# Kernel tuning notes

Measured on AMD Instinct MI355X. Metric: run time of the kernel, lower is better.

The kernel has to match this reference:

```python
import jax, jax.numpy as jnp
import numpy as np
from itertools import combinations

# Static conv hyperparameters (match init_kwargs)
KH = KW = 3
SH = SW = 1
PH = PW = 1
DH = DW = 1
MAJ_DIM = 3  # = kernel_size[0]


def _maj_sim(x):
    """Vectorized bipolar majority-gate simulation. x: [B, n] -> [B].
    result = sum over majority subsets of prod((1+x)_in, (1-x)_out) / 2^(n-1) - 1
    """
    n = x.shape[1]
    thresh = (n + 1) // 2
    one_plus = 1.0 + x
    one_minus = 1.0 - x
    res = jnp.zeros(x.shape[0], dtype=x.dtype)
    for k in range(thresh, n + 1):
        for combo in combinations(range(n), k):
            mask = np.zeros(n, dtype=bool)
            mask[list(combo)] = True
            res = res + jnp.prod(jnp.where(jnp.asarray(mask), one_plus, one_minus), axis=1)
    return res / (2.0 ** (n - 1)) - 1.0


def _stack_maj_sim(x, maj_dim):
    """Stacked majority tree reduction along dim 1. x: [B, n] -> [B, n_final]."""
    B = x.shape[0]
    while x.shape[1] >= maj_dim:
        num_chunks = x.shape[1] // maj_dim
        if num_chunks == 0:
            break
        z = x[:, : num_chunks * maj_dim].reshape(B * num_chunks, maj_dim)
        x = _maj_sim(z).reshape(B, num_chunks)
    return x


def _unfold(x):
    """torch.nn.functional.unfold equivalent. x:[N,C,H,W] -> [N, C*KH*KW, L].
    Feature ordering matches torch: c-major, then kernel row, then kernel col."""
    N, C, H, W = x.shape
    H_out = (H + 2 * PH - DH * (KH - 1) - 1) // SH + 1
    W_out = (W + 2 * PW - DW * (KW - 1) - 1) // SW + 1
    xp = jnp.pad(x, ((0, 0), (0, 0), (PH, PH), (PW, PW)))
    slabs = [
        xp[:, :, i * DH : i * DH + SH * (H_out - 1) + 1 : SH,
              j * DW : j * DW + SW * (W_out - 1) + 1 : SW]
        for i in range(KH) for j in range(KW)
    ]
    p = jnp.stack(slabs, axis=2)  # [N, C, KH*KW, H_out, W_out]
    return p.reshape(N, C * KH * KW, H_out * W_out)


def setup_inputs() -> dict:
    key = jax.random.key(0)
    k1, k2 = jax.random.split(key)
    x = jax.random.normal(k1, (2, 27, 64, 64), dtype=jnp.float32)
    # kaiming-uniform-ish scale for fan_in = 27*3*3 = 243
    weight = jax.random.normal(k2, (32, 27, 3, 3), dtype=jnp.float32) * 0.06
    return {"x": x, "weight": weight}


def reference(x, weight):
    N, C, H, W = x.shape
    OC = weight.shape[0]
    H_out = (H + 2 * PH - DH * (KH - 1) - 1) // SH + 1
    W_out = (W + 2 * PW - DW * (KW - 1) - 1) // SW + 1
    patches = _unfold(x)                       # [N, F, L], F = C*KH*KW
    weight_flat = weight.reshape(OC, -1)       # [OC, F]
    # prod: [N, OC, F, L]
    prod = patches[:, None, :, :] * weight_flat[None, :, :, None]
    F_ = prod.shape[2]
    L = prod.shape[3]
    # reduce the feature dim via stacked majority simulation
    z = prod.transpose(0, 1, 3, 2).reshape(N * OC * L, F_)
    out = _stack_maj_sim(z, MAJ_DIM)           # [N*OC*L, 1]
    return out.reshape(N, OC, H_out, W_out)
```

## Files before the change

### kernel.cpp

```cpp
#include <hip/hip_runtime.h>

#define TW 16
#define TH 16
#define CIN 27
#define HH 64
#define WW 64
#define OC 32

__device__ __forceinline__ float maj3(float a, float b, float c) {
    return 0.5f * (a + b + c - a * b * c);
}

__global__ __launch_bounds__(256) void sconv_maj_kernel(
    const float* __restrict__ x,
    const float* __restrict__ wgt,
    float* __restrict__ out)
{
    __shared__ float sx[CIN][TH + 2][TW + 2];
    __shared__ float sw[CIN * 9];

    const int tx = threadIdx.x;
    const int ty = threadIdx.y;
    const int tid = ty * TW + tx;
    const int tile_w0 = blockIdx.x * TW;
    const int tile_h0 = blockIdx.y * TH;
    const int noc = blockIdx.z;
    const int n  = noc >> 5;
    const int oc = noc & 31;

    if (tid < CIN * 9)
        sw[tid] = wgt[oc * (CIN * 9) + tid];

    const int TOT = CIN * (TH + 2) * (TW + 2);
    const float* xn = x + (size_t)n * (CIN * HH * WW);
    for (int idx = tid; idx < TOT; idx += TH * TW) {
        int c   = idx / ((TH + 2) * (TW + 2));
        int rem = idx - c * ((TH + 2) * (TW + 2));
        int r   = rem / (TW + 2);
        int col = rem - r * (TW + 2);
        int gr = tile_h0 + r - 1;
        int gc = tile_w0 + col - 1;
        float v = 0.0f;
        if (gr >= 0 && gr < HH && gc >= 0 && gc < WW)
            v = xn[c * (HH * WW) + gr * WW + gc];
        ((float*)sx)[idx] = v;
    }
    __syncthreads();

    float m2[CIN];
    #pragma unroll
    for (int c = 0; c < CIN; ++c) {
        float m1[3];
        #pragma unroll
        for (int ki = 0; ki < 3; ++ki) {
            float p0 = sx[c][ty + ki][tx + 0] * sw[c * 9 + ki * 3 + 0];
            float p1 = sx[c][ty + ki][tx + 1] * sw[c * 9 + ki * 3 + 1];
            float p2 = sx[c][ty + ki][tx + 2] * sw[c * 9 + ki * 3 + 2];
            m1[ki] = maj3(p0, p1, p2);
        }
        m2[c] = maj3(m1[0], m1[1], m1[2]);
    }
    float m3[9];
    #pragma unroll
    for (int g = 0; g < 9; ++g)
        m3[g] = maj3(m2[3 * g], m2[3 * g + 1], m2[3 * g + 2]);
    float m4a = maj3(m3[0], m3[1], m3[2]);
    float m4b = maj3(m3[3], m3[4], m3[5]);
    float m4c = maj3(m3[6], m3[7], m3[8]);
    float res = maj3(m4a, m4b, m4c);

    const int h = tile_h0 + ty;
    const int w = tile_w0 + tx;
    out[(((size_t)n * OC + oc) * HH + h) * WW + w] = res;
}

extern "C" void kernel_launch(void* const* d_in, const int* in_sizes, int n_in,
                              void* d_out, int out_size, void* d_ws, size_t ws_size,
                              hipStream_t stream) {
    const float* x   = (const float*)d_in[0];
    const float* wgt = (const float*)d_in[1];
    float* out = (float*)d_out;

    dim3 block(TW, TH, 1);
    dim3 grid(WW / TW, HH / TH, 2 * OC);
    sconv_maj_kernel<<<grid, block, 0, stream>>>(x, wgt, out);
}
```

Before: 84.47 us.

## Compute two adjacent outputs per thread with float2 loads and direct weight reads

Each thread now computes two horizontally adjacent outputs, so the block shrinks to 128 threads. Overlapping window values are reused from float2 shared-memory loads and the result is written with one float2 store. Weights are read straight from global memory (uniform across the block, likely scalar loads) instead of being staged in shared memory. The aim is fewer LDS reads per output and less work per output. The cost is more registers per thread (float2 m2[27]) and half as many threads per block, which lowers latency hiding. The float2 read of prow[tx+1] at row offset 2*tx+2 relies on an even row stride of 18 floats for alignment, which holds.

```diff
diff --git a/kernel.cpp b/kernel.cpp
--- a/kernel.cpp
+++ b/kernel.cpp
@@ -1,39 +1,37 @@
 #include <hip/hip_runtime.h>
 
-#define TW 16
-#define TH 16
 #define CIN 27
 #define HH 64
 #define WW 64
 #define OC 32
+#define TW 16
+#define TH 16
 
-__device__ __forceinline__ float maj3(float a, float b, float c) {
-    return 0.5f * (a + b + c - a * b * c);
+__device__ __forceinline__ float2 pk_maj3(float2 a, float2 b, float2 c) {
+    float2 r;
+    r.x = 0.5f * (a.x + b.x + c.x - a.x * b.x * c.x);
+    r.y = 0.5f * (a.y + b.y + c.y - a.y * b.y * c.y);
+    return r;
 }
 
-__global__ __launch_bounds__(256) void sconv_maj_kernel(
+__global__ __launch_bounds__(128) void sconv_maj_kernel(
     const float* __restrict__ x,
     const float* __restrict__ wgt,
     float* __restrict__ out)
 {
     __shared__ float sx[CIN][TH + 2][TW + 2];
-    __shared__ float sw[CIN * 9];
 
     const int tx = threadIdx.x;
     const int ty = threadIdx.y;
-    const int tid = ty * TW + tx;
+    const int tid = ty * 8 + tx;
     const int tile_w0 = blockIdx.x * TW;
     const int tile_h0 = blockIdx.y * TH;
-    const int noc = blockIdx.z;
-    const int n  = noc >> 5;
-    const int oc = noc & 31;
-
-    if (tid < CIN * 9)
-        sw[tid] = wgt[oc * (CIN * 9) + tid];
+    const int n  = blockIdx.z >> 5;
+    const int oc = blockIdx.z & 31;
 
     const int TOT = CIN * (TH + 2) * (TW + 2);
     const float* xn = x + (size_t)n * (CIN * HH * WW);
-    for (int idx = tid; idx < TOT; idx += TH * TW) {
+    for (int idx = tid; idx < TOT; idx += 128) {
         int c   = idx / ((TH + 2) * (TW + 2));
         int rem = idx - c * ((TH + 2) * (TW + 2));
         int r   = rem / (TW + 2);
@@ -47,31 +45,40 @@
     }
     __syncthreads();
 
-    float m2[CIN];
+    const float* __restrict__ wb = wgt + oc * (CIN * 9);
+
+    float2 m2[CIN];
     #pragma unroll
     for (int c = 0; c < CIN; ++c) {
-        float m1[3];
+        float2 m1[3];
         #pragma unroll
         for (int ki = 0; ki < 3; ++ki) {
-            float p0 = sx[c][ty + ki][tx + 0] * sw[c * 9 + ki * 3 + 0];
-            float p1 = sx[c][ty + ki][tx + 1] * sw[c * 9 + ki * 3 + 1];
-            float p2 = sx[c][ty + ki][tx + 2] * sw[c * 9 + ki * 3 + 2];
-            m1[ki] = maj3(p0, p1, p2);
+            const float2* prow = (const float2*)(&sx[c][ty + ki][0]);
+            float2 v01 = prow[tx];
+            float2 v23 = prow[tx + 1];
+            float w0 = wb[c * 9 + ki * 3 + 0];
+            float w1 = wb[c * 9 + ki * 3 + 1];
+            float w2 = wb[c * 9 + ki * 3 + 2];
+            float2 p0 = make_float2(v01.x * w0, v01.y * w0);
+            float2 p1 = make_float2(v01.y * w1, v23.x * w1);
+            float2 p2 = make_float2(v23.x * w2, v23.y * w2);
+            m1[ki] = pk_maj3(p0, p1, p2);
         }
-        m2[c] = maj3(m1[0], m1[1], m1[2]);
+        m2[c] = pk_maj3(m1[0], m1[1], m1[2]);
     }
-    float m3[9];
+    float2 m3[9];
     #pragma unroll
     for (int g = 0; g < 9; ++g)
-        m3[g] = maj3(m2[3 * g], m2[3 * g + 1], m2[3 * g + 2]);
-    float m4a = maj3(m3[0], m3[1], m3[2]);
-    float m4b = maj3(m3[3], m3[4], m3[5]);
-    float m4c = maj3(m3[6], m3[7], m3[8]);
-    float res = maj3(m4a, m4b, m4c);
+        m3[g] = pk_maj3(m2[3 * g], m2[3 * g + 1], m2[3 * g + 2]);
+    float2 m4a = pk_maj3(m3[0], m3[1], m3[2]);
+    float2 m4b = pk_maj3(m3[3], m3[4], m3[5]);
+    float2 m4c = pk_maj3(m3[6], m3[7], m3[8]);
+    float2 res = pk_maj3(m4a, m4b, m4c);
 
     const int h = tile_h0 + ty;
-    const int w = tile_w0 + tx;
-    out[(((size_t)n * OC + oc) * HH + h) * WW + w] = res;
+    const int w = tile_w0 + 2 * tx;
+    float2* po = (float2*)(out + (((size_t)n * OC + oc) * HH + h) * WW + w);
+    *po = res;
 }
 
 extern "C" void kernel_launch(void* const* d_in, const int* in_sizes, int n_in,
@@ -81,7 +88,7 @@
     const float* wgt = (const float*)d_in[1];
     float* out = (float*)d_out;
 
-    dim3 block(TW, TH, 1);
+    dim3 block(8, 16, 1);
     dim3 grid(WW / TW, HH / TH, 2 * OC);
     sconv_maj_kernel<<<grid, block, 0, stream>>>(x, wgt, out);
 }
```

Result: slower. 88.39 us (+4.6%).
